# Kernel tuning notes

Hardware: AMD Instinct MI355X
Metric: run time of the kernel (lower is better)

The kernel has to match this reference:

```python
import jax, jax.numpy as jnp
import numpy as np

D_MODEL = 1024
NUM_HEADS = 16
D_K = D_MODEL // NUM_HEADS
B, S = 2, 2048


def setup_inputs() -> dict:
    key = jax.random.key(0)
    ks = jax.random.split(key, 11)
    sc = 1.0 / np.sqrt(D_MODEL)
    return {
        "Q_input": jax.random.normal(ks[0], (B, S, D_MODEL), jnp.float32),
        "K_input": jax.random.normal(ks[1], (B, S, D_MODEL), jnp.float32),
        "V_input": jax.random.normal(ks[2], (B, S, D_MODEL), jnp.float32),
        "Wq": jax.random.normal(ks[3], (D_MODEL, D_MODEL), jnp.float32) * sc,
        "bq": jax.random.normal(ks[4], (D_MODEL,), jnp.float32) * 0.01,
        "Wk": jax.random.normal(ks[5], (D_MODEL, D_MODEL), jnp.float32) * sc,
        "bk": jax.random.normal(ks[6], (D_MODEL,), jnp.float32) * 0.01,
        "Wv": jax.random.normal(ks[7], (D_MODEL, D_MODEL), jnp.float32) * sc,
        "bv": jax.random.normal(ks[8], (D_MODEL,), jnp.float32) * 0.01,
        "Wo": jax.random.normal(ks[9], (D_MODEL, D_MODEL), jnp.float32) * sc,
        "bo": jax.random.normal(ks[10], (D_MODEL,), jnp.float32) * 0.01,
    }


def reference(Q_input, K_input, V_input, Wq, bq, Wk, bk, Wv, bv, Wo, bo):
    # Linear projections (torch Linear: x @ W.T + b)
    Q = Q_input @ Wq.T + bq  # [B,S,D]
    K = K_input @ Wk.T + bk
    V = V_input @ Wv.T + bv
    # split heads -> [B,H,S,dk]
    def split(x):
        return x.reshape(B, S, NUM_HEADS, D_K).transpose(0, 2, 1, 3)
    Qh, Kh, Vh = split(Q), split(K), split(V)
    scale = 1.0 / jnp.sqrt(jnp.asarray(D_K, Qh.dtype))
    scores = jnp.einsum('bhqd,bhkd->bhqk', Qh, Kh) * scale  # [B,H,S,S]
    attn = jax.nn.softmax(scores, axis=-1)
    ctx = jnp.einsum('bhqk,bhkd->bhqd', attn, Vh)  # [B,H,S,dk]
    concat = ctx.transpose(0, 2, 1, 3).reshape(B, S, D_MODEL)
    out = concat @ Wo.T + bo  # dropout is identity in eval
    return out
```

## Files before the change

kernel.cpp:

```cpp
#include <hip/hip_runtime.h>
#include <stdint.h>

#define DM   1024
#define NH   16
#define DKH  64
#define BBATCH 2
#define SEQ  2048
#define MTOK (BBATCH*SEQ)

typedef unsigned short u16;
typedef unsigned int   u32;
typedef __attribute__((ext_vector_type(8))) short  bf16x8;
typedef __attribute__((ext_vector_type(4))) float  f32x4;

struct PtrArr11 { const void* p[11]; };
struct U16Arr11 { u16* p[11]; };

__device__ __forceinline__ float bf2f(u16 u) {
  union { unsigned int i; float f; } z; z.i = ((unsigned int)u) << 16; return z.f;
}
__device__ __forceinline__ u16 f2bf(float f) {
  union { float f; unsigned int i; } z; z.f = f;
  unsigned int i = z.i + 0x7fffu + ((z.i >> 16) & 1u);
  return (u16)(i >> 16);
}

__device__ __forceinline__ bf16x8 u4_to_bf(u32 a, u32 b, u32 c, u32 d) {
  union { u32 u[4]; bf16x8 v; } z; z.u[0] = a; z.u[1] = b; z.u[2] = c; z.u[3] = d; return z.v;
}

__device__ __forceinline__ void gld16(const void* g, void* l) {
  __builtin_amdgcn_global_load_lds(
      (const __attribute__((address_space(1))) void*)g,
      (__attribute__((address_space(3))) void*)l,
      16, 0, 0);
}

__global__ void k_detect(const unsigned int* __restrict__ w, int* __restrict__ flag) {
  const int ln = threadIdx.x & 63;
  const unsigned int word = w[ln];
  const unsigned int ex = (word >> 7) & 0xFFu;
  const int hit = (ex >= 100u && ex <= 126u) ? 1 : 0;
  unsigned long long m = __ballot(hit);
  if (ln == 0) *flag = (__popcll(m) >= 40) ? 0 : 1;
}

__global__ __launch_bounds__(256) void k_convert_all(PtrArr11 src, U16Arr11 dst,
                                                     const int* __restrict__ flag) {
  if (*flag == 0) return;
  const int b = blockIdx.x;
  int seg, base;
  if      (b <  2048) { seg = 0;  base = 0;    }
  else if (b <  4096) { seg = 1;  base = 2048; }
  else if (b <  6144) { seg = 2;  base = 4096; }
  else if (b <  6656) { seg = 3;  base = 6144; }
  else if (b == 6656) { seg = 4;  base = 6656; }
  else if (b <  7169) { seg = 5;  base = 6657; }
  else if (b == 7169) { seg = 6;  base = 7169; }
  else if (b <  7682) { seg = 7;  base = 7170; }
  else if (b == 7682) { seg = 8;  base = 7682; }
  else if (b <  8195) { seg = 9;  base = 7683; }
  else                { seg = 10; base = 8195; }
  const int n = (seg < 3) ? (MTOK * DM) : ((seg & 1) ? (DM * DM) : DM);
  const int i0 = (b - base) * 2048 + threadIdx.x * 8;
  if (i0 >= n) return;
  const float* s = (const float*)src.p[seg] + i0;
  const f32x4 x0 = *(const f32x4*)(s);
  const f32x4 x1 = *(const f32x4*)(s + 4);
  bf16x8 o;
#pragma unroll
  for (int j = 0; j < 4; ++j) o[j] = (short)f2bf(x0[j]);
#pragma unroll
  for (int j = 0; j < 4; ++j) o[4 + j] = (short)f2bf(x1[j]);
  *(bf16x8*)(dst.p[seg] + i0) = o;
}

__device__ __forceinline__ void gemm_body64(const u16* __restrict__ X,
                                            const u16* __restrict__ W,
                                            const u16* __restrict__ bias,
                                            u16* __restrict__ out)
{
  __shared__ __attribute__((aligned(16))) u16 sA[128 * 64];
  __shared__ __attribute__((aligned(16))) u16 sB[128 * 64];
  const int tid = threadIdx.x;
  const int ln = tid & 63, wv = tid >> 6;
  const int wm = wv & 1, wn = wv >> 1;
  const int m0 = blockIdx.y * 128, n0 = blockIdx.x * 128;
  const int fr = ln & 15, fq = ln >> 4;
  const int fr7 = fr & 7;
  const int srow = ln >> 3;
  const int scol = ((ln & 7) ^ srow) * 8;

  f32x4 acc[4][4];
#pragma unroll
  for (int i = 0; i < 4; ++i)
#pragma unroll
    for (int j = 0; j < 4; ++j) acc[i][j] = (f32x4){0.f, 0.f, 0.f, 0.f};

  const u16* pA = X + (size_t)(m0 + wv * 32 + srow) * DM + scol;
  const u16* pB = W + (size_t)(n0 + wv * 32 + srow) * DM + scol;
  u16* lA = sA + wv * 32 * 64;
  u16* lB = sB + wv * 32 * 64;

  for (int k0 = 0; k0 < DM; k0 += 64) {
#pragma unroll
    for (int c = 0; c < 4; ++c) {
      gld16(pA + (size_t)(c * 8) * DM + k0, lA + c * 8 * 64);
      gld16(pB + (size_t)(c * 8) * DM + k0, lB + c * 8 * 64);
    }
    asm volatile("s_waitcnt vmcnt(0)" ::: "memory");
    __syncthreads();

    bf16x8 af[4][2], bfg[4][2];
#pragma unroll
    for (int t = 0; t < 4; ++t)
#pragma unroll
      for (int ks = 0; ks < 2; ++ks) {
        af[t][ks]  = *(const bf16x8*)(sA + (wm * 64 + t * 16 + fr) * 64 + ((ks * 4 + fq) ^ fr7) * 8);
        bfg[t][ks] = *(const bf16x8*)(sB + (wn * 64 + t * 16 + fr) * 64 + ((ks * 4 + fq) ^ fr7) * 8);
      }
#pragma unroll
    for (int i = 0; i < 4; ++i)
#pragma unroll
      for (int j = 0; j < 4; ++j) {
        acc[i][j] = __builtin_amdgcn_mfma_f32_16x16x32_bf16(af[i][0], bfg[j][0], acc[i][j], 0, 0, 0);
        acc[i][j] = __builtin_amdgcn_mfma_f32_16x16x32_bf16(af[i][1], bfg[j][1], acc[i][j], 0, 0, 0);
      }
    __syncthreads();
  }

#pragma unroll
  for (int i = 0; i < 4; ++i) {
    const int row = m0 + wm * 64 + i * 16 + fq * 4;
#pragma unroll
    for (int j = 0; j < 4; ++j) {
      const int col = n0 + wn * 64 + j * 16 + fr;
      const float bv = bf2f(bias[col]);
#pragma unroll
      for (int r = 0; r < 4; ++r)
        out[(size_t)(row + r) * DM + col] = f2bf(acc[i][j][r] + bv);
    }
  }
}

__device__ __forceinline__ void gemm_body_n64(const u16* __restrict__ X,
                                              const u16* __restrict__ W,
                                              const u16* __restrict__ bias,
                                              void* __restrict__ out,
                                              int isf32out)
{
  __shared__ __attribute__((aligned(16))) u16 sA[128 * 32];
  __shared__ __attribute__((aligned(16))) u16 sB[64 * 32];
  const int tid = threadIdx.x;
  const int ln = tid & 63, wv = tid >> 6;
  const int wm = wv >> 1, wn = wv & 1;
  const int m0 = blockIdx.y * 128, n0 = blockIdx.x * 64;
  const int fr = ln & 15, fq = ln >> 4;
  const int srow = ln >> 2, sslot = (ln & 3) * 8;

  f32x4 acc[4][2];
#pragma unroll
  for (int i = 0; i < 4; ++i)
#pragma unroll
    for (int j = 0; j < 2; ++j) acc[i][j] = (f32x4){0.f, 0.f, 0.f, 0.f};

  const u16* pA = X + (size_t)(m0 + wv * 32 + srow) * DM + sslot;
  const u16* pB = W + (size_t)(n0 + wv * 16 + srow) * DM + sslot;
  u16* lA0 = sA + (wv * 2) * 512; u16* lA1 = sA + (wv * 2 + 1) * 512;
  u16* lB  = sB + wv * 512;

  for (int k0 = 0; k0 < DM; k0 += 32) {
    gld16(pA + k0,           lA0);
    gld16(pA + 16 * DM + k0, lA1);
    gld16(pB + k0,           lB);
    asm volatile("s_waitcnt vmcnt(0)" ::: "memory");
    __syncthreads();

    bf16x8 af[4], bfg[2];
#pragma unroll
    for (int t = 0; t < 4; ++t)
      af[t]  = *(const bf16x8*)(sA + (wm * 64 + t * 16 + fr) * 32 + fq * 8);
#pragma unroll
    for (int t = 0; t < 2; ++t)
      bfg[t] = *(const bf16x8*)(sB + (wn * 32 + t * 16 + fr) * 32 + fq * 8);
#pragma unroll
    for (int i = 0; i < 4; ++i)
#pragma unroll
      for (int j = 0; j < 2; ++j)
        acc[i][j] = __builtin_amdgcn_mfma_f32_16x16x32_bf16(af[i], bfg[j], acc[i][j], 0, 0, 0);
    __syncthreads();
  }

#pragma unroll
  for (int i = 0; i < 4; ++i) {
    const int row = m0 + wm * 64 + i * 16 + fq * 4;
#pragma unroll
    for (int j = 0; j < 2; ++j) {
      const int col = n0 + wn * 32 + j * 16 + fr;
      const float bv = bf2f(bias[col]);
#pragma unroll
      for (int r = 0; r < 4; ++r) {
        const float val = acc[i][j][r] + bv;
        const size_t idx = (size_t)(row + r) * DM + col;
        if (isf32out) ((float*)out)[idx] = val;
        else          ((u16*)out)[idx]   = f2bf(val);
      }
    }
  }
}

__global__ __launch_bounds__(256, 2) void k_gemm_qkv(
    PtrArr11 orig, U16Arr11 conv, const int* __restrict__ flag,
    u16* oq, u16* ok, u16* ov)
{
  const int f = *flag;
  const int z = blockIdx.z;
  const u16* X  = f ? conv.p[z]         : (const u16*)orig.p[z];
  const u16* W  = f ? conv.p[3 + 2 * z] : (const u16*)orig.p[3 + 2 * z];
  const u16* bi = f ? conv.p[4 + 2 * z] : (const u16*)orig.p[4 + 2 * z];
  u16* o = (z == 0) ? oq : (z == 1) ? ok : ov;
  gemm_body64(X, W, bi, o);
}

__global__ __launch_bounds__(256, 2) void k_gemm_one(
    const u16* X, const void* Wo_o, const u16* Wo_c,
    const void* bo_o, const u16* bo_c, const int* __restrict__ flag, void* o)
{
  const int f = *flag;
  const u16* W  = f ? Wo_c : (const u16*)Wo_o;
  const u16* bi = f ? bo_c : (const u16*)bo_o;
  gemm_body_n64(X, W, bi, o, f);
}

__global__ __launch_bounds__(256) void k_transpose(const u16* __restrict__ in,
                                                   u16* __restrict__ out)
{
  __shared__ u16 t[64][66];
  const int b = blockIdx.z;
  const int s0 = blockIdx.x * 64, d0 = blockIdx.y * 64;
  const int c = threadIdx.x & 63, r0 = threadIdx.x >> 6;
#pragma unroll
  for (int i = 0; i < 16; ++i) {
    const int r = r0 + 4 * i;
    t[r][c] = in[(size_t)(b * SEQ + s0 + r) * DM + d0 + c];
  }
  __syncthreads();
#pragma unroll
  for (int i = 0; i < 16; ++i) {
    const int r = r0 + 4 * i;
    out[(size_t)(b * DM + d0 + r) * SEQ + s0 + c] = t[c][r];
  }
}

__global__ __launch_bounds__(256, 2) void k_attn(
    const u16* __restrict__ Qp, const u16* __restrict__ Kp,
    const u16* __restrict__ Vt, u16* __restrict__ ctx)
{
  __shared__ __attribute__((aligned(16))) u16 sK[2][64 * 64];
  __shared__ __attribute__((aligned(16))) u16 sV[2][64 * 64];

  const int tid = threadIdx.x;
  const int ln = tid & 63, wv = tid >> 6;
  const int bid = blockIdx.y * 16 + blockIdx.x;
  const int bh  = ((bid >> 7) << 3) | (bid & 7);
  const int qx  = (bid >> 3) & 15;
  const int b = bh >> 4, h = bh & 15;
  const int q0 = qx * 128 + wv * 32;
  const int fr = ln & 15, fq = ln >> 4;
  const int fr7 = fr & 7;

  const int srow = ln >> 3;
  const int scol = ((ln & 7) ^ srow) * 8;
  const u16* gK0 = Kp + (size_t)(b * SEQ + wv * 16 + srow) * DM + h * DKH + scol;
  const u16* gV0 = Vt + (size_t)(b * DM + h * DKH + wv * 16 + srow) * SEQ + scol;
  u16* sKb = &sK[0][0];
  u16* sVb = &sV[0][0];

  bf16x8 qf[2][2];
#pragma unroll
  for (int qt = 0; qt < 2; ++qt)
#pragma unroll
    for (int ks = 0; ks < 2; ++ks) {
      const u16* src = Qp + (size_t)(b * SEQ + q0 + qt * 16 + fr) * DM + h * DKH + ks * 32 + fq * 8;
      bf16x8 v = *(const bf16x8*)src;
      bf16x8 w;
#pragma unroll
      for (int j = 0; j < 8; ++j) w[j] = (short)f2bf(bf2f((u16)v[j]) * 0.125f);
      qf[qt][ks] = w;
    }

  float l_a[2] = {0.f, 0.f};
  float l_b[2] = {0.f, 0.f};
  f32x4 o_acc[2][4];
#pragma unroll
  for (int qt = 0; qt < 2; ++qt)
#pragma unroll
    for (int dt = 0; dt < 4; ++dt) o_acc[qt][dt] = (f32x4){0.f, 0.f, 0.f, 0.f};

#define STAGE_KV(pp, key0)                                     \
  do {                                                         \
    u16* kd = sKb + (pp) * 4096 + wv * 1024;                   \
    u16* vd = sVb + (pp) * 4096 + wv * 1024;                   \
    gld16(gK0 + (size_t)(key0) * DM, kd);                      \
    gld16(gK0 + (size_t)((key0) + 8) * DM, kd + 512);          \
    gld16(gV0 + (key0), vd);                                   \
    gld16(gV0 + (key0) + 8 * SEQ, vd + 512);                   \
  } while (0)

  STAGE_KV(0, 0);
  asm volatile("s_waitcnt vmcnt(0)" ::: "memory");
  __syncthreads();

  int p = 0;
  for (int kb = 0; kb < SEQ / 64; ++kb) {
    if (kb + 1 < SEQ / 64) STAGE_KV(p ^ 1, (kb + 1) * 64);

    const u16* K = sKb + p * 4096;
    const u16* V = sVb + p * 4096;

    bf16x8 kf[4][2];
#pragma unroll
    for (int nt = 0; nt < 4; ++nt)
#pragma unroll
      for (int ks = 0; ks < 2; ++ks)
        kf[nt][ks] = *(const bf16x8*)(K + (nt * 16 + fr) * 64 + ((ks * 4 + fq) ^ fr7) * 8);

    u32 pw[2][2][4];
#pragma unroll
    for (int qt = 0; qt < 2; ++qt) {
      f32x4 s_acc[4];
#pragma unroll
      for (int nt = 0; nt < 4; ++nt) s_acc[nt] = (f32x4){0.f, 0.f, 0.f, 0.f};
      __builtin_amdgcn_s_setprio(1);
#pragma unroll
      for (int nt = 0; nt < 4; ++nt)
#pragma unroll
        for (int ks = 0; ks < 2; ++ks)
          s_acc[nt] = __builtin_amdgcn_mfma_f32_16x16x32_bf16(kf[nt][ks], qf[qt][ks], s_acc[nt], 0, 0, 0);
      __builtin_amdgcn_s_setprio(0);

      u32 w[4][2];
#pragma unroll
      for (int nt = 0; nt < 4; ++nt)
#pragma unroll
        for (int t = 0; t < 2; ++t) {
          const float e0 = __expf(s_acc[nt][2 * t]);
          const float e1 = __expf(s_acc[nt][2 * t + 1]);
          l_a[qt] += e0;
          l_b[qt] += e1;
          u32 wd;
          asm("v_cvt_pk_bf16_f32 %0, %1, %2" : "=v"(wd) : "v"(e0), "v"(e1));
          w[nt][t] = wd;
        }
#pragma unroll
      for (int ks = 0; ks < 2; ++ks) {
        u32 a0 = w[2 * ks][0], b0 = w[2 * ks + 1][0];
        u32 a1 = w[2 * ks][1], b1 = w[2 * ks + 1][1];
        asm("v_permlane32_swap_b32 %0, %1" : "+v"(a0), "+v"(b0));
        asm("v_permlane16_swap_b32 %0, %1" : "+v"(a0), "+v"(b0));
        asm("v_permlane32_swap_b32 %0, %1" : "+v"(a1), "+v"(b1));
        asm("v_permlane16_swap_b32 %0, %1" : "+v"(a1), "+v"(b1));
        pw[qt][ks][0] = a0; pw[qt][ks][1] = a1; pw[qt][ks][2] = b0; pw[qt][ks][3] = b1;
      }
    }

#pragma unroll
    for (int dt = 0; dt < 4; ++dt) {
      bf16x8 vf0 = *(const bf16x8*)(V + (dt * 16 + fr) * 64 + ((0 + fq) ^ fr7) * 8);
      bf16x8 vf1 = *(const bf16x8*)(V + (dt * 16 + fr) * 64 + ((4 + fq) ^ fr7) * 8);
      __builtin_amdgcn_s_setprio(1);
#pragma unroll
      for (int qt = 0; qt < 2; ++qt) {
        o_acc[qt][dt] = __builtin_amdgcn_mfma_f32_16x16x32_bf16(
            u4_to_bf(pw[qt][0][0], pw[qt][0][1], pw[qt][0][2], pw[qt][0][3]), vf0, o_acc[qt][dt], 0, 0, 0);
        o_acc[qt][dt] = __builtin_amdgcn_mfma_f32_16x16x32_bf16(
            u4_to_bf(pw[qt][1][0], pw[qt][1][1], pw[qt][1][2], pw[qt][1][3]), vf1, o_acc[qt][dt], 0, 0, 0);
      }
      __builtin_amdgcn_s_setprio(0);
    }

    asm volatile("s_waitcnt vmcnt(0)" ::: "memory");
    __syncthreads();
    p ^= 1;
  }
#undef STAGE_KV

  float iv[2][4];
#pragma unroll
  for (int qt = 0; qt < 2; ++qt) {
    float t = l_a[qt] + l_b[qt];
    t += __shfl_xor(t, 16);
    t += __shfl_xor(t, 32);
    const float rl = 1.0f / t;
#pragma unroll
    for (int rr = 0; rr < 4; ++rr) iv[qt][rr] = __shfl(rl, fq * 4 + rr);
  }
#pragma unroll
  for (int qt = 0; qt < 2; ++qt)
#pragma unroll
    for (int dt = 0; dt < 4; ++dt)
#pragma unroll
      for (int r = 0; r < 4; ++r) {
        const int qrow = q0 + qt * 16 + fq * 4 + r;
        const int col = h * DKH + dt * 16 + fr;
        ctx[(size_t)(b * SEQ + qrow) * DM + col] = f2bf(o_acc[qt][dt][r] * iv[qt][r]);
      }
}

extern "C" void kernel_launch(void* const* d_in, const int* in_sizes, int n_in,
                              void* d_out, int out_size, void* d_ws, size_t ws_size,
                              hipStream_t stream)
{
  char* ws = (char*)d_ws;
  int* flag = (int*)ws;

  const size_t TOKSZ = (size_t)MTOK * DM * sizeof(u16);
  const size_t WSZ   = (size_t)DM * DM * sizeof(u16);
  const size_t BSZ   = 4096;

  size_t off = 256;
  u16* Qc  = (u16*)(ws + off); off += TOKSZ;
  u16* Kc  = (u16*)(ws + off); off += TOKSZ;
  u16* Vc  = (u16*)(ws + off); off += TOKSZ;
  u16* Wqc = (u16*)(ws + off); off += WSZ;
  u16* Wkc = (u16*)(ws + off); off += WSZ;
  u16* Wvc = (u16*)(ws + off); off += WSZ;
  u16* Woc = (u16*)(ws + off); off += WSZ;
  u16* bqc = (u16*)(ws + off); off += BSZ;
  u16* bkc = (u16*)(ws + off); off += BSZ;
  u16* bvc = (u16*)(ws + off); off += BSZ;
  u16* boc = (u16*)(ws + off); off += BSZ;
  u16* Qp  = (u16*)(ws + off); off += TOKSZ;
  u16* Kp  = (u16*)(ws + off); off += TOKSZ;
  u16* Vp  = (u16*)(ws + off); off += TOKSZ;
  u16* Vt  = Qc;
  u16* ctx = Kc;

  PtrArr11 orig;
  for (int i = 0; i < 11; ++i) orig.p[i] = d_in[i];
  U16Arr11 conv;
  conv.p[0] = Qc;  conv.p[1] = Kc;  conv.p[2] = Vc;
  conv.p[3] = Wqc; conv.p[4] = bqc; conv.p[5] = Wkc; conv.p[6] = bkc;
  conv.p[7] = Wvc; conv.p[8] = bvc; conv.p[9] = Woc; conv.p[10] = boc;

  dim3 blk(256);

  k_detect<<<1, 64, 0, stream>>>((const unsigned int*)d_in[3], flag);
  k_convert_all<<<8196, blk, 0, stream>>>(orig, conv, flag);
  k_gemm_qkv<<<dim3(DM / 128, MTOK / 128, 3), blk, 0, stream>>>(
      orig, conv, flag, Qp, Kp, Vp);
  k_transpose<<<dim3(SEQ / 64, DM / 64, BBATCH), blk, 0, stream>>>(Vp, Vt);
  k_attn<<<dim3(SEQ / 128, BBATCH * NH), blk, 0, stream>>>(Qp, Kp, Vt, ctx);
  k_gemm_one<<<dim3(DM / 64, MTOK / 128, 1), blk, 0, stream>>>(
      ctx, d_in[9], Woc, d_in[10], boc, flag, d_out);
}
```

Before: 229.5 us.

## Stage 128 keys per attention iteration and swizzle GEMM block order

The attention kernel now loads and processes 128 keys per loop iteration instead of 64, in two 64-key halves. This halves the number of wait-and-barrier points and gives each prefetch more compute to hide behind, at the cost of doubling K/V shared memory to 64KB per block, which can reduce occupancy. Both projection GEMMs also remap the block index so groups of consecutive blocks cover nearby M tiles at the same N tile, meant to improve L2 reuse of the weight and activation tiles.

```diff
diff --git a/kernel.cpp b/kernel.cpp
--- a/kernel.cpp
+++ b/kernel.cpp
@@ -78,14 +78,14 @@
 __device__ __forceinline__ void gemm_body64(const u16* __restrict__ X,
                                             const u16* __restrict__ W,
                                             const u16* __restrict__ bias,
-                                            u16* __restrict__ out)
+                                            u16* __restrict__ out,
+                                            int m0, int n0)
 {
   __shared__ __attribute__((aligned(16))) u16 sA[128 * 64];
   __shared__ __attribute__((aligned(16))) u16 sB[128 * 64];
   const int tid = threadIdx.x;
   const int ln = tid & 63, wv = tid >> 6;
   const int wm = wv & 1, wn = wv >> 1;
-  const int m0 = blockIdx.y * 128, n0 = blockIdx.x * 128;
   const int fr = ln & 15, fq = ln >> 4;
   const int fr7 = fr & 7;
   const int srow = ln >> 3;
@@ -147,14 +147,13 @@
                                               const u16* __restrict__ W,
                                               const u16* __restrict__ bias,
                                               void* __restrict__ out,
-                                              int isf32out)
+                                              int isf32out, int m0, int n0)
 {
   __shared__ __attribute__((aligned(16))) u16 sA[128 * 32];
   __shared__ __attribute__((aligned(16))) u16 sB[64 * 32];
   const int tid = threadIdx.x;
   const int ln = tid & 63, wv = tid >> 6;
   const int wm = wv >> 1, wn = wv & 1;
-  const int m0 = blockIdx.y * 128, n0 = blockIdx.x * 64;
   const int fr = ln & 15, fq = ln >> 4;
   const int srow = ln >> 2, sslot = (ln & 3) * 8;
 
@@ -219,7 +218,10 @@
   const u16* W  = f ? conv.p[3 + 2 * z] : (const u16*)orig.p[3 + 2 * z];
   const u16* bi = f ? conv.p[4 + 2 * z] : (const u16*)orig.p[4 + 2 * z];
   u16* o = (z == 0) ? oq : (z == 1) ? ok : ov;
-  gemm_body64(X, W, bi, o);
+  const int bid = blockIdx.y * 8 + blockIdx.x;
+  const int m0 = ((((bid >> 3) & 3) << 3) | (bid & 7)) * 128;
+  const int n0 = (bid >> 5) * 128;
+  gemm_body64(X, W, bi, o, m0, n0);
 }
 
 __global__ __launch_bounds__(256, 2) void k_gemm_one(
@@ -229,7 +231,10 @@
   const int f = *flag;
   const u16* W  = f ? Wo_c : (const u16*)Wo_o;
   const u16* bi = f ? bo_c : (const u16*)bo_o;
-  gemm_body_n64(X, W, bi, o, f);
+  const int bid = blockIdx.y * 16 + blockIdx.x;
+  const int m0 = ((((bid >> 3) & 3) << 3) | (bid & 7)) * 128;
+  const int n0 = ((bid >> 5) & 15) * 64;
+  gemm_body_n64(X, W, bi, o, f, m0, n0);
 }
 
 __global__ __launch_bounds__(256) void k_transpose(const u16* __restrict__ in,
@@ -256,8 +261,8 @@
     const u16* __restrict__ Qp, const u16* __restrict__ Kp,
     const u16* __restrict__ Vt, u16* __restrict__ ctx)
 {
-  __shared__ __attribute__((aligned(16))) u16 sK[2][64 * 64];
-  __shared__ __attribute__((aligned(16))) u16 sV[2][64 * 64];
+  __shared__ __attribute__((aligned(16))) u16 sK[2][2][64 * 64];
+  __shared__ __attribute__((aligned(16))) u16 sV[2][2][64 * 64];
 
   const int tid = threadIdx.x;
   const int ln = tid & 63, wv = tid >> 6;
@@ -273,8 +278,8 @@
   const int scol = ((ln & 7) ^ srow) * 8;
   const u16* gK0 = Kp + (size_t)(b * SEQ + wv * 16 + srow) * DM + h * DKH + scol;
   const u16* gV0 = Vt + (size_t)(b * DM + h * DKH + wv * 16 + srow) * SEQ + scol;
-  u16* sKb = &sK[0][0];
-  u16* sVb = &sV[0][0];
+  u16* sKb = &sK[0][0][0];
+  u16* sVb = &sV[0][0][0];
 
   bf16x8 qf[2][2];
 #pragma unroll
@@ -297,93 +302,100 @@
 #pragma unroll
     for (int dt = 0; dt < 4; ++dt) o_acc[qt][dt] = (f32x4){0.f, 0.f, 0.f, 0.f};
 
-#define STAGE_KV(pp, key0)                                     \
-  do {                                                         \
-    u16* kd = sKb + (pp) * 4096 + wv * 1024;                   \
-    u16* vd = sVb + (pp) * 4096 + wv * 1024;                   \
-    gld16(gK0 + (size_t)(key0) * DM, kd);                      \
-    gld16(gK0 + (size_t)((key0) + 8) * DM, kd + 512);          \
-    gld16(gV0 + (key0), vd);                                   \
-    gld16(gV0 + (key0) + 8 * SEQ, vd + 512);                   \
+#define STAGE_KV128(pp, key0)                                       \
+  do {                                                              \
+    _Pragma("unroll")                                               \
+    for (int hh = 0; hh < 2; ++hh) {                                \
+      u16* kd = sKb + (pp) * 8192 + hh * 4096 + wv * 1024;          \
+      u16* vd = sVb + (pp) * 8192 + hh * 4096 + wv * 1024;          \
+      const int kk = (key0) + hh * 64;                              \
+      gld16(gK0 + (size_t)kk * DM, kd);                             \
+      gld16(gK0 + (size_t)(kk + 8) * DM, kd + 512);                 \
+      gld16(gV0 + kk, vd);                                          \
+      gld16(gV0 + kk + 8 * SEQ, vd + 512);                          \
+    }                                                               \
   } while (0)
 
-  STAGE_KV(0, 0);
+  STAGE_KV128(0, 0);
   asm volatile("s_waitcnt vmcnt(0)" ::: "memory");
   __syncthreads();
 
   int p = 0;
-  for (int kb = 0; kb < SEQ / 64; ++kb) {
-    if (kb + 1 < SEQ / 64) STAGE_KV(p ^ 1, (kb + 1) * 64);
-
-    const u16* K = sKb + p * 4096;
-    const u16* V = sVb + p * 4096;
-
-    bf16x8 kf[4][2];
-#pragma unroll
-    for (int nt = 0; nt < 4; ++nt)
-#pragma unroll
-      for (int ks = 0; ks < 2; ++ks)
-        kf[nt][ks] = *(const bf16x8*)(K + (nt * 16 + fr) * 64 + ((ks * 4 + fq) ^ fr7) * 8);
-
-    u32 pw[2][2][4];
-#pragma unroll
-    for (int qt = 0; qt < 2; ++qt) {
-      f32x4 s_acc[4];
-#pragma unroll
-      for (int nt = 0; nt < 4; ++nt) s_acc[nt] = (f32x4){0.f, 0.f, 0.f, 0.f};
-      __builtin_amdgcn_s_setprio(1);
+  for (int kb = 0; kb < SEQ / 128; ++kb) {
+    if (kb + 1 < SEQ / 128) STAGE_KV128(p ^ 1, (kb + 1) * 128);
+
+#pragma unroll
+    for (int hh = 0; hh < 2; ++hh) {
+      const u16* K = sKb + p * 8192 + hh * 4096;
+      const u16* V = sVb + p * 8192 + hh * 4096;
+
+      bf16x8 kf[4][2];
 #pragma unroll
       for (int nt = 0; nt < 4; ++nt)
 #pragma unroll
         for (int ks = 0; ks < 2; ++ks)
-          s_acc[nt] = __builtin_amdgcn_mfma_f32_16x16x32_bf16(kf[nt][ks], qf[qt][ks], s_acc[nt], 0, 0, 0);
-      __builtin_amdgcn_s_setprio(0);
-
-      u32 w[4][2];
-#pragma unroll
-      for (int nt = 0; nt < 4; ++nt)
-#pragma unroll
-        for (int t = 0; t < 2; ++t) {
-          const float e0 = __expf(s_acc[nt][2 * t]);
-          const float e1 = __expf(s_acc[nt][2 * t + 1]);
-          l_a[qt] += e0;
-          l_b[qt] += e1;
-          u32 wd;
-          asm("v_cvt_pk_bf16_f32 %0, %1, %2" : "=v"(wd) : "v"(e0), "v"(e1));
-          w[nt][t] = wd;
+          kf[nt][ks] = *(const bf16x8*)(K + (nt * 16 + fr) * 64 + ((ks * 4 + fq) ^ fr7) * 8);
+
+      u32 pw[2][2][4];
+#pragma unroll
+      for (int qt = 0; qt < 2; ++qt) {
+        f32x4 s_acc[4];
+#pragma unroll
+        for (int nt = 0; nt < 4; ++nt) s_acc[nt] = (f32x4){0.f, 0.f, 0.f, 0.f};
+        __builtin_amdgcn_s_setprio(1);
+#pragma unroll
+        for (int nt = 0; nt < 4; ++nt)
+#pragma unroll
+          for (int ks = 0; ks < 2; ++ks)
+            s_acc[nt] = __builtin_amdgcn_mfma_f32_16x16x32_bf16(kf[nt][ks], qf[qt][ks], s_acc[nt], 0, 0, 0);
+        __builtin_amdgcn_s_setprio(0);
+
+        u32 w[4][2];
+#pragma unroll
+        for (int nt = 0; nt < 4; ++nt)
+#pragma unroll
+          for (int t = 0; t < 2; ++t) {
+            const float e0 = __expf(s_acc[nt][2 * t]);
+            const float e1 = __expf(s_acc[nt][2 * t + 1]);
+            l_a[qt] += e0;
+            l_b[qt] += e1;
+            u32 wd;
+            asm("v_cvt_pk_bf16_f32 %0, %1, %2" : "=v"(wd) : "v"(e0), "v"(e1));
+            w[nt][t] = wd;
+          }
+#pragma unroll
+        for (int ks = 0; ks < 2; ++ks) {
+          u32 a0 = w[2 * ks][0], b0 = w[2 * ks + 1][0];
+          u32 a1 = w[2 * ks][1], b1 = w[2 * ks + 1][1];
+          asm("v_permlane32_swap_b32 %0, %1" : "+v"(a0), "+v"(b0));
+          asm("v_permlane16_swap_b32 %0, %1" : "+v"(a0), "+v"(b0));
+          asm("v_permlane32_swap_b32 %0, %1" : "+v"(a1), "+v"(b1));
+          asm("v_permlane16_swap_b32 %0, %1" : "+v"(a1), "+v"(b1));
+          pw[qt][ks][0] = a0; pw[qt][ks][1] = a1; pw[qt][ks][2] = b0; pw[qt][ks][3] = b1;
         }
-#pragma unroll
-      for (int ks = 0; ks < 2; ++ks) {
-        u32 a0 = w[2 * ks][0], b0 = w[2 * ks + 1][0];
-        u32 a1 = w[2 * ks][1], b1 = w[2 * ks + 1][1];
-        asm("v_permlane32_swap_b32 %0, %1" : "+v"(a0), "+v"(b0));
-        asm("v_permlane16_swap_b32 %0, %1" : "+v"(a0), "+v"(b0));
-        asm("v_permlane32_swap_b32 %0, %1" : "+v"(a1), "+v"(b1));
-        asm("v_permlane16_swap_b32 %0, %1" : "+v"(a1), "+v"(b1));
-        pw[qt][ks][0] = a0; pw[qt][ks][1] = a1; pw[qt][ks][2] = b0; pw[qt][ks][3] = b1;
-      }
-    }
-
-#pragma unroll
-    for (int dt = 0; dt < 4; ++dt) {
-      bf16x8 vf0 = *(const bf16x8*)(V + (dt * 16 + fr) * 64 + ((0 + fq) ^ fr7) * 8);
-      bf16x8 vf1 = *(const bf16x8*)(V + (dt * 16 + fr) * 64 + ((4 + fq) ^ fr7) * 8);
-      __builtin_amdgcn_s_setprio(1);
-#pragma unroll
-      for (int qt = 0; qt < 2; ++qt) {
-        o_acc[qt][dt] = __builtin_amdgcn_mfma_f32_16x16x32_bf16(
-            u4_to_bf(pw[qt][0][0], pw[qt][0][1], pw[qt][0][2], pw[qt][0][3]), vf0, o_acc[qt][dt], 0, 0, 0);
-        o_acc[qt][dt] = __builtin_amdgcn_mfma_f32_16x16x32_bf16(
-            u4_to_bf(pw[qt][1][0], pw[qt][1][1], pw[qt][1][2], pw[qt][1][3]), vf1, o_acc[qt][dt], 0, 0, 0);
-      }
-      __builtin_amdgcn_s_setprio(0);
+      }
+
+#pragma unroll
+      for (int dt = 0; dt < 4; ++dt) {
+        bf16x8 vf0 = *(const bf16x8*)(V + (dt * 16 + fr) * 64 + ((0 + fq) ^ fr7) * 8);
+        bf16x8 vf1 = *(const bf16x8*)(V + (dt * 16 + fr) * 64 + ((4 + fq) ^ fr7) * 8);
+        __builtin_amdgcn_s_setprio(1);
+#pragma unroll
+        for (int qt = 0; qt < 2; ++qt) {
+          o_acc[qt][dt] = __builtin_amdgcn_mfma_f32_16x16x32_bf16(
+              u4_to_bf(pw[qt][0][0], pw[qt][0][1], pw[qt][0][2], pw[qt][0][3]), vf0, o_acc[qt][dt], 0, 0, 0);
+          o_acc[qt][dt] = __builtin_amdgcn_mfma_f32_16x16x32_bf16(
+              u4_to_bf(pw[qt][1][0], pw[qt][1][1], pw[qt][1][2], pw[qt][1][3]), vf1, o_acc[qt][dt], 0, 0, 0);
+        }
+        __builtin_amdgcn_s_setprio(0);
+      }
     }
 
     asm volatile("s_waitcnt vmcnt(0)" ::: "memory");
     __syncthreads();
     p ^= 1;
   }
-#undef STAGE_KV
+#undef STAGE_KV128
 
   float iv[2][4];
 #pragma unroll
```

Measured after the change: 220.6 us. 3.9% less time.
